# Kernel tuning notes

Measured on AMD Instinct MI355X. Metric: run time of the kernel, lower is better.

The kernel has to match this reference:

```python
import jax, jax.numpy as jnp
import numpy as np

B, N, H, L, V = 512, 20, 450, 56, 780
T = 2 * (N - 1)  # DFS trace length per tree (down+up edge per non-root node)


def _build(rng):
    EpT = 2 * (N - 1)
    n_nodes, n_edges = B * N, B * EpT
    src = np.zeros(n_edges, np.int32); dst = np.zeros(n_edges, np.int32)
    step_eid = np.zeros((T, B), np.int32)
    step_v = np.zeros((T, B), np.int32)
    p_flag = np.zeros((T, B), np.int32)
    for b in range(B):
        par = [0] * N
        ch = [[] for _ in range(N)]
        for i in range(1, N):
            p = int(rng.integers(max(0, i - 3), i))
            par[i] = p; ch[p].append(i)
        eo, no = b * EpT, b * N
        for i in range(1, N):
            d, u = eo + 2 * (i - 1), eo + 2 * (i - 1) + 1
            src[d], dst[d] = no + par[i], no + i
            src[u], dst[u] = no + i, no + par[i]
        trace = []
        stack = [(0, iter(ch[0]))]
        while stack:
            u_, it = stack[-1]
            c = next(it, None)
            if c is None:
                stack.pop()
                if stack:
                    pu = stack[-1][0]
                    trace.append((eo + 2 * (u_ - 1) + 1, no + pu, 0))
            else:
                trace.append((eo + 2 * (c - 1), no + c, 1))
                stack.append((c, iter(ch[c])))
        for t, (e, v, p) in enumerate(trace):
            step_eid[t, b], step_v[t, b], p_flag[t, b] = e, v, p
    return src, dst, step_eid, step_v, p_flag


def setup_inputs() -> dict:
    rng = np.random.default_rng(0)
    src, dst, step_eid, step_v, p_flag = _build(rng)
    n_nodes, n_edges = B * N, B * 2 * (N - 1)
    in_lists = [[] for _ in range(n_nodes)]
    for e in range(n_edges):
        in_lists[dst[e]].append(e)
    Dn = max(len(l) for l in in_lists)
    node_in = np.full((n_nodes, Dn), n_edges, np.int32)  # pad with sentinel n_edges
    for v, l in enumerate(in_lists):
        node_in[v, :len(l)] = l
    # line-graph (non-backtracking) predecessors of edge e=(u,v): edges (w,u), w != v
    preds = [[e2 for e2 in in_lists[src[e]] if src[e2] != dst[e]] for e in range(n_edges)]
    P = max(1, max(len(l) for l in preds))
    edge_pred = np.full((n_edges, P), n_edges, np.int32)
    for e, l in enumerate(preds):
        edge_pred[e, :len(l)] = l
    wid = rng.integers(0, V, n_nodes).astype(np.int32)
    root_ids = (np.arange(B) * N).astype(np.int32)
    # q rows: root block, then per-step rows where node is new (down edges)
    q_rows = list(range(B)); q_tgt = [int(wid[r]) for r in root_ids]
    for t in range(T):
        for b in range(B):
            if p_flag[t, b]:
                q_rows.append((t + 1) * B + b)
                q_tgt.append(int(wid[step_v[t, b]]))
    p_tgt = np.concatenate([p_flag.reshape(-1), np.zeros(B, np.int32)]).astype(np.int32)
    key = jax.random.key(0)
    def W(k, *shape):
        return jax.random.normal(jax.random.fold_in(key, k), shape, jnp.float32) * 0.05
    return dict(
        tree_vec=W(0, B, L), emb=W(1, V, H),
        Wz=W(2, 2 * H, H), bz=jnp.zeros(H, jnp.float32),
        Wh=W(3, 2 * H, H), bh=jnp.zeros(H, jnp.float32),
        Wr=W(4, H, H), Ur=W(5, H, H), br=jnp.zeros(H, jnp.float32),
        Ww=W(6, H + L, H), bw=jnp.zeros(H, jnp.float32),
        Uw=W(7, 2 * H + L, H), bu=jnp.zeros(H, jnp.float32),
        Wo=W(8, H, V), bo=jnp.zeros(V, jnp.float32),
        Us=W(9, H, 1), bs=jnp.zeros(1, jnp.float32),
        wid=jnp.asarray(wid), root_ids=jnp.asarray(root_ids),
        edge_src=jnp.asarray(src), edge_dst=jnp.asarray(dst),
        edge_pred=jnp.asarray(edge_pred), node_in=jnp.asarray(node_in),
        step_eid=jnp.asarray(step_eid), step_v=jnp.asarray(step_v),
        q_rows=jnp.asarray(np.array(q_rows, np.int32)),
        q_tgt=jnp.asarray(np.array(q_tgt, np.int32)),
        p_tgt=jnp.asarray(p_tgt),
    )


def reference(tree_vec, emb, Wz, bz, Wh, bh, Wr, Ur, br, Ww, bw, Uw, bu, Wo, bo, Us, bs,
              wid, root_ids, edge_src, edge_dst, edge_pred, node_in, step_eid, step_v,
              q_rows, q_tgt, p_tgt):
    n_edges = edge_src.shape[0]
    x = emb[wid]                              # [n_nodes, H] node embeddings
    src_x = x[edge_src]; dst_x = x[edge_dst]  # [n_edges, H]
    m0 = jnp.zeros((n_edges + 1, H), x.dtype)  # +1 sentinel zero row for padding

    def step(carry, inp):
        m, rm = carry
        eid, v = inp                          # [B] edge ids / dst node ids this DFS step
        pred = edge_pred[eid]                 # [B, P] non-backtracking predecessor edges
        s = m[pred].sum(1)                    # sum of incoming m
        arm = rm[pred].sum(1)                 # sum of incoming r*m
        sx = src_x[eid]; dx = dst_x[eid]
        z = jax.nn.sigmoid(jnp.concatenate([sx, s], 1) @ Wz + bz)
        m_new = (1 - z) * s + z * jnp.tanh(jnp.concatenate([sx, arm], 1) @ Wh + bh)
        r = jax.nn.sigmoid(dx @ Wr + m_new @ Ur + br)
        m = m.at[eid].set(m_new)
        rm = rm.at[eid].set(r * m_new)
        h = m[node_in[v]].sum(1)              # node pull: h_v = sum of incoming m
        return (m, rm), h

    _, h_steps = jax.lax.scan(step, (m0, m0), (step_eid, step_v))  # [T, B, H]

    x_root = x[root_ids]
    h_root = jnp.zeros_like(x_root)           # roots pulled before any edge update
    x_steps = x[step_v]                        # [T, B, H]
    tv_steps = jnp.broadcast_to(tree_vec[None], (T, B, L))
    p_root = jnp.concatenate([x_root, h_root, tree_vec], 1)[None]
    p_step = jnp.concatenate([x_steps, h_steps, tv_steps], 2)
    p_in = jnp.concatenate([p_root, p_step], 0).reshape((T + 1) * B, 2 * H + L)
    q_root = jnp.concatenate([h_root, tree_vec], 1)[None]
    q_step = jnp.concatenate([h_steps, tv_steps], 2)
    q_in = jnp.concatenate([q_root, q_step], 0).reshape((T + 1) * B, H + L)[q_rows]

    q_logits = jax.nn.relu(q_in @ Ww + bw) @ Wo + bo          # [nq, V]
    p_logit = (jax.nn.relu(p_in @ Uw + bu) @ Us + bs)[:, 0]   # [np]
    tgt = p_tgt.astype(p_logit.dtype)
    p_loss = jnp.sum(jnp.logaddexp(0.0, p_logit) - p_logit * tgt) / B
    lse = jax.nn.logsumexp(q_logits, axis=1)
    q_loss = jnp.sum(lse - jnp.take_along_axis(q_logits, q_tgt[:, None], 1)[:, 0]) / B
    p_acc = jnp.mean(((p_logit > 0).astype(p_tgt.dtype) == p_tgt).astype(jnp.float32))
    q_acc = jnp.mean((jnp.argmax(q_logits, 1).astype(q_tgt.dtype) == q_tgt).astype(jnp.float32))
    return (q_loss, p_loss, q_acc, p_acc)
```

## Files before the change

kernel.cpp:

```cpp
#include <hip/hip_runtime.h>
#include <math.h>

#define B_ 512
#define N_ 20
#define H_ 450
#define L_ 56
#define V_ 780
#define T_ 38
#define NNODES (B_*N_)
#define NEDGES (B_*2*(N_-1))
#define NPROWS ((T_+1)*B_)
#define KS 480
#define NT 4
#define AST 488
#define HSTR 456

typedef __attribute__((ext_vector_type(8))) short bf16x8;
typedef __attribute__((ext_vector_type(4))) float f32x4;

__device__ __forceinline__ float sigmoidf_(float v){ return 1.0f/(1.0f+expf(-v)); }

__device__ __forceinline__ unsigned short f2b(float x){
  unsigned int u = __float_as_uint(x);
  unsigned int r = (u + 0x7fffu + ((u >> 16) & 1u)) >> 16;
  return (unsigned short)r;
}
__device__ __forceinline__ float b2f(unsigned int v){
  return __uint_as_float((v & 0xffffu) << 16);
}
__device__ __forceinline__ unsigned int pack2(float lo, float hi){
  return (unsigned int)f2b(lo) | ((unsigned int)f2b(hi) << 16);
}

__global__ __launch_bounds__(256) void k_gather_xb(const float* __restrict__ emb,
    const int* __restrict__ wid, unsigned short* __restrict__ xb){
  int w = blockIdx.x*4 + (threadIdx.x>>6), lane = threadIdx.x & 63;
  if (w >= NNODES) return;
  const float2* src = (const float2*)(emb + (size_t)wid[w]*H_);
  unsigned int* dst = (unsigned int*)(xb + (size_t)w*KS);
  for (int j2 = lane; j2 < 240; j2 += 64){
    unsigned int v = 0;
    if (j2 < 225){ float2 f = src[j2]; v = pack2(f.x, f.y); }
    dst[j2] = v;
  }
}

__global__ void k_wt(const float* __restrict__ W1, const float* __restrict__ W2,
                     int Ksplit, int Kact, int Nact, unsigned short* __restrict__ dst, int Kpad){
  int c = blockIdx.x;
  unsigned short* drow = dst + (size_t)c*Kpad;
  for (int k = threadIdx.x; k < Kpad; k += blockDim.x){
    float v = 0.f;
    if (c < Nact && k < Kact)
      v = (k < Ksplit) ? W1[(size_t)k*Nact + c] : W2[(size_t)(k-Ksplit)*Nact + c];
    drow[k] = f2b(v);
  }
}

struct ScanP {
  const unsigned short *WzB, *WhB, *UrT;
  const unsigned short *XWz, *XWh, *XWr;
  const int *edge_src, *edge_dst, *step_eid;
  unsigned short *m, *rm;
  unsigned short *hm, *hrm;
  unsigned short *hb;
};

__global__ __launch_bounds__(1024, 4) void k_scan_tree(ScanP p){
  __shared__ unsigned short A1s[16*AST];
  __shared__ unsigned short A2s[16*AST];
  __shared__ unsigned short sZ[NT*HSTR], sH[NT*HSTR], sR[NT*HSTR];
  __shared__ int s_eoff[T_][NT], s_roff[T_][NT], s_srcH[T_][NT], s_dstH[T_][NT];

  const int tid = threadIdx.x;
  const int lane = tid & 63, l15 = lane & 15, kh = lane >> 4, ko = kh*8;
  const int wv = tid >> 6;
  const int r0 = blockIdx.x * NT;
  const int c_0 = wv*32 + l15, c_1 = c_0 + 16;

  const unsigned short* pWz0 = p.WzB + (size_t)c_0*KS;
  const unsigned short* pWz1 = p.WzB + (size_t)c_1*KS;
  const unsigned short* pWh0 = p.WhB + (size_t)c_0*KS;
  const unsigned short* pWh1 = p.WhB + (size_t)c_1*KS;
  const unsigned short* pUr0 = p.UrT + (size_t)c_0*KS;
  const unsigned short* pUr1 = p.UrT + (size_t)c_1*KS;
  const unsigned short* aA1 = A1s + l15*AST;
  const unsigned short* aA2 = A2s + l15*AST;

  for (int idx = tid; idx < 16*AST; idx += 1024){ A1s[idx] = 0; A2s[idx] = 0; }
  for (int idx = tid; idx < T_*NT; idx += 1024){
    int t = idx >> 2, rl = idx & 3;
    int e = p.step_eid[t*B_ + r0 + rl];
    s_eoff[t][rl] = e*KS;
    s_roff[t][rl] = (e ^ 1)*KS;
    s_srcH[t][rl] = p.edge_src[e]*HSTR;
    s_dstH[t][rl] = p.edge_dst[e]*HSTR;
  }
  __syncthreads();

  for (int t = 0; t < T_; ++t){
    bf16x8 bz0[3], bz1[3], bh0[3], bh1[3];
    #pragma unroll
    for (int i = 0; i < 3; ++i){
      bz0[i] = *(const bf16x8*)(pWz0 + i*32 + ko);
      bz1[i] = *(const bf16x8*)(pWz1 + i*32 + ko);
      bh0[i] = *(const bf16x8*)(pWh0 + i*32 + ko);
      bh1[i] = *(const bf16x8*)(pWh1 + i*32 + ko);
    }

    if (tid < 228){
      int rl = tid / 57, g = tid - rl*57;
      int j = g*8;
      uint4 hm4 = *(const uint4*)(p.hm  + s_srcH[t][rl] + j);
      uint4 hr4 = *(const uint4*)(p.hrm + s_srcH[t][rl] + j);
      uint4 mr4 = *(const uint4*)(p.m   + s_roff[t][rl] + j);
      uint4 rr4 = *(const uint4*)(p.rm  + s_roff[t][rl] + j);
      uint4 o1, o2;
      o1.x = pack2(b2f(hm4.x)-b2f(mr4.x), b2f(hm4.x>>16)-b2f(mr4.x>>16));
      o1.y = pack2(b2f(hm4.y)-b2f(mr4.y), b2f(hm4.y>>16)-b2f(mr4.y>>16));
      o1.z = pack2(b2f(hm4.z)-b2f(mr4.z), b2f(hm4.z>>16)-b2f(mr4.z>>16));
      o1.w = pack2(b2f(hm4.w)-b2f(mr4.w), b2f(hm4.w>>16)-b2f(mr4.w>>16));
      o2.x = pack2(b2f(hr4.x)-b2f(rr4.x), b2f(hr4.x>>16)-b2f(rr4.x>>16));
      o2.y = pack2(b2f(hr4.y)-b2f(rr4.y), b2f(hr4.y>>16)-b2f(rr4.y>>16));
      o2.z = pack2(b2f(hr4.z)-b2f(rr4.z), b2f(hr4.z>>16)-b2f(rr4.z>>16));
      o2.w = pack2(b2f(hr4.w)-b2f(rr4.w), b2f(hr4.w>>16)-b2f(rr4.w>>16));
      *(uint4*)(A1s + rl*AST + j) = o1;
      *(uint4*)(A2s + rl*AST + j) = o2;
    } else if (tid < 912){
      int idx2 = tid - 228;
      int mat = idx2 / 228, rem = idx2 - mat*228;
      int rl = rem / 57, g = rem - rl*57;
      int row = (mat == 2) ? s_dstH[t][rl] : s_srcH[t][rl];
      const unsigned short* src = (mat == 0) ? p.XWz : (mat == 1) ? p.XWh : p.XWr;
      unsigned short* d = (mat == 0) ? sZ : (mat == 1) ? sH : sR;
      *(uint4*)(d + rl*HSTR + g*8) = *(const uint4*)(src + row + g*8);
    }
    __syncthreads();

    f32x4 accZ0 = {}, accZ1 = {}, accH0 = {}, accH1 = {};
    #pragma unroll
    for (int it = 0; it < 15; ++it){
      const int sl = it % 3;
      bf16x8 a1 = *(const bf16x8*)(aA1 + it*32 + ko);
      bf16x8 a2 = *(const bf16x8*)(aA2 + it*32 + ko);
      accZ0 = __builtin_amdgcn_mfma_f32_16x16x32_bf16(a1, bz0[sl], accZ0, 0,0,0);
      accZ1 = __builtin_amdgcn_mfma_f32_16x16x32_bf16(a1, bz1[sl], accZ1, 0,0,0);
      accH0 = __builtin_amdgcn_mfma_f32_16x16x32_bf16(a2, bh0[sl], accH0, 0,0,0);
      accH1 = __builtin_amdgcn_mfma_f32_16x16x32_bf16(a2, bh1[sl], accH1, 0,0,0);
      if (it + 3 < 15){
        bz0[sl] = *(const bf16x8*)(pWz0 + (it+3)*32 + ko);
        bz1[sl] = *(const bf16x8*)(pWz1 + (it+3)*32 + ko);
        bh0[sl] = *(const bf16x8*)(pWh0 + (it+3)*32 + ko);
        bh1[sl] = *(const bf16x8*)(pWh1 + (it+3)*32 + ko);
      }
    }
    __syncthreads();

    bf16x8 bu0[3], bu1[3];
    #pragma unroll
    for (int i = 0; i < 3; ++i){
      bu0[i] = *(const bf16x8*)(pUr0 + i*32 + ko);
      bu1[i] = *(const bf16x8*)(pUr1 + i*32 + ko);
    }

    if (kh == 0){
      #pragma unroll
      for (int n = 0; n < 2; ++n){
        int cc = wv*32 + n*16 + l15;
        if (cc < H_){
          f32x4 aZ = n ? accZ1 : accZ0;
          f32x4 aH = n ? accH1 : accH0;
          #pragma unroll
          for (int reg = 0; reg < 4; ++reg){
            int rl = reg;
            float z  = sigmoidf_(aZ[reg] + b2f(sZ[rl*HSTR + cc]));
            float th = tanhf   (aH[reg] + b2f(sH[rl*HSTR + cc]));
            float s_ = b2f(A1s[rl*AST + cc]);
            float mn = (1.f - z)*s_ + z*th;
            unsigned short mb = f2b(mn);
            p.m[s_eoff[t][rl] + cc] = mb;
            A2s[rl*AST + cc] = mb;
            float hv = b2f(p.hm[s_dstH[t][rl] + cc]) + mn;
            p.hm[s_dstH[t][rl] + cc] = f2b(hv);
            p.hb[(size_t)(t*B_ + r0 + rl)*HSTR + cc] = f2b(hv);
          }
        }
      }
    }
    __syncthreads();

    f32x4 accR0 = {}, accR1 = {};
    #pragma unroll
    for (int it = 0; it < 15; ++it){
      const int sl = it % 3;
      bf16x8 a = *(const bf16x8*)(aA2 + it*32 + ko);
      accR0 = __builtin_amdgcn_mfma_f32_16x16x32_bf16(a, bu0[sl], accR0, 0,0,0);
      accR1 = __builtin_amdgcn_mfma_f32_16x16x32_bf16(a, bu1[sl], accR1, 0,0,0);
      if (it + 3 < 15){
        bu0[sl] = *(const bf16x8*)(pUr0 + (it+3)*32 + ko);
        bu1[sl] = *(const bf16x8*)(pUr1 + (it+3)*32 + ko);
      }
    }

    if (kh == 0){
      #pragma unroll
      for (int n = 0; n < 2; ++n){
        int cc = wv*32 + n*16 + l15;
        if (cc < H_){
          f32x4 aR = n ? accR1 : accR0;
          #pragma unroll
          for (int reg = 0; reg < 4; ++reg){
            int rl = reg;
            float r_ = sigmoidf_(aR[reg] + b2f(sR[rl*HSTR + cc]));
            float mn = b2f(A2s[rl*AST + cc]);
            float rv = r_*mn;
            p.rm[s_eoff[t][rl] + cc] = f2b(rv);
            float hv = b2f(p.hrm[s_dstH[t][rl] + cc]) + rv;
            p.hrm[s_dstH[t][rl] + cc] = f2b(hv);
          }
        }
      }
    }
    __syncthreads();
  }
}

__device__ __forceinline__ void mfma_tile_core(
    const unsigned short* __restrict__ A, const unsigned short* __restrict__ BT,
    int K, int gr0, int gc0, int tid,
    unsigned short* __restrict__ As, unsigned short* __restrict__ Bs,
    f32x4 (&acc)[2][2])
{
  const int lane = tid & 63;
  const int w = tid >> 6, wr = w >> 1, wc = w & 1;
  const int l15 = lane & 15, kh = lane >> 4;
  const int sr = tid >> 2, sj = (tid & 3) * 8;
  const size_t arow = (size_t)(gr0 + sr) * K;
  const size_t brow = (size_t)(gc0 + sr) * K;
  for (int kt = 0; kt < K; kt += 32){
    __syncthreads();
    *(float4*)&As[sr*40 + sj] = *(const float4*)&A[arow + kt + sj];
    *(float4*)&Bs[sr*40 + sj] = *(const float4*)&BT[brow + kt + sj];
    __syncthreads();
    bf16x8 a0 = *(const bf16x8*)&As[(wr*32      + l15)*40 + kh*8];
    bf16x8 a1 = *(const bf16x8*)&As[(wr*32 + 16 + l15)*40 + kh*8];
    bf16x8 b0 = *(const bf16x8*)&Bs[(wc*32      + l15)*40 + kh*8];
    bf16x8 b1 = *(const bf16x8*)&Bs[(wc*32 + 16 + l15)*40 + kh*8];
    acc[0][0] = __builtin_amdgcn_mfma_f32_16x16x32_bf16(a0,b0,acc[0][0],0,0,0);
    acc[0][1] = __builtin_amdgcn_mfma_f32_16x16x32_bf16(a0,b1,acc[0][1],0,0,0);
    acc[1][0] = __builtin_amdgcn_mfma_f32_16x16x32_bf16(a1,b0,acc[1][0],0,0,0);
    acc[1][1] = __builtin_amdgcn_mfma_f32_16x16x32_bf16(a1,b1,acc[1][1],0,0,0);
  }
}

__global__ __launch_bounds__(256) void k_head_mfma(
    const unsigned short* __restrict__ A, const unsigned short* __restrict__ BT, int K,
    const float* __restrict__ bias, int Nact, int relu,
    float* __restrict__ outF, int ldF, unsigned short* __restrict__ outB, int ldB)
{
  __shared__ unsigned short As[64*40], Bs[64*40];
  const int tid = threadIdx.x;
  const int gr0 = blockIdx.y*64, gc0 = blockIdx.x*64;
  f32x4 acc[2][2] = {};
  mfma_tile_core(A, BT, K, gr0, gc0, tid, As, Bs, acc);
  const int lane = tid & 63;
  const int w = tid >> 6, wr = w >> 1, wc = w & 1;
  const int l15 = lane & 15, kh = lane >> 4;
  #pragma unroll
  for (int mi = 0; mi < 2; ++mi){
    #pragma unroll
    for (int n = 0; n < 2; ++n){
      int c = gc0 + wc*32 + n*16 + l15;
      float bc = (c < Nact) ? bias[c] : 0.f;
      #pragma unroll
      for (int reg = 0; reg < 4; ++reg){
        int r = gr0 + wr*32 + mi*16 + kh*4 + reg;
        float v = acc[mi][n][reg] + bc;
        if (relu) v = fmaxf(v, 0.f);
        if (outF && c < Nact) outF[(size_t)r*ldF + c] = v;
        if (outB && c < ldB)  outB[(size_t)r*ldB + c] = (c < Nact) ? f2b(v) : (unsigned short)0;
      }
    }
  }
}

__global__ __launch_bounds__(256) void k_head_p(
    const unsigned short* __restrict__ A, const unsigned short* __restrict__ BT,
    const float* __restrict__ bu_, const float* __restrict__ Us, float* __restrict__ plog)
{
  __shared__ unsigned short As[64*40], Bs[64*40];
  const int tid = threadIdx.x;
  const int gr0 = blockIdx.y*64, gc0 = blockIdx.x*64;
  f32x4 acc[2][2] = {};
  mfma_tile_core(A, BT, 960, gr0, gc0, tid, As, Bs, acc);
  const int lane = tid & 63;
  const int w = tid >> 6, wr = w >> 1, wc = w & 1;
  const int l15 = lane & 15, kh = lane >> 4;
  #pragma unroll
  for (int mi = 0; mi < 2; ++mi){
    float rowsum[4] = {0.f,0.f,0.f,0.f};
    #pragma unroll
    for (int n = 0; n < 2; ++n){
      int c = gc0 + wc*32 + n*16 + l15;
      float uc = 0.f, bc = 0.f;
      if (c < H_){ uc = Us[c]; bc = bu_[c]; }
      #pragma unroll
      for (int reg = 0; reg < 4; ++reg){
        float v = fmaxf(acc[mi][n][reg] + bc, 0.f);
        rowsum[reg] += (c < H_) ? v*uc : 0.f;
      }
    }
    #pragma unroll
    for (int reg = 0; reg < 4; ++reg){
      float pv = rowsum[reg];
      pv += __shfl_xor(pv,1); pv += __shfl_xor(pv,2);
      pv += __shfl_xor(pv,4); pv += __shfl_xor(pv,8);
      if (l15 == 0) atomicAdd(plog + gr0 + wr*32 + mi*16 + kh*4 + reg, pv);
    }
  }
}

__global__ __launch_bounds__(256) void k_build_Aq(const unsigned short* __restrict__ hb,
    const float* __restrict__ tv, const int* __restrict__ q_rows,
    unsigned short* __restrict__ Aq, int nq){
  int w = blockIdx.x*4 + (threadIdx.x>>6), lane = threadIdx.x & 63;
  int nw = gridDim.x*4;
  for (int i = w; i < nq; i += nw){
    int row = q_rows[i]; int b = row & (B_-1);
    unsigned short* dst = Aq + (size_t)i*512;
    if (row < B_){
      for (int j2 = lane; j2 < 225; j2 += 64) ((unsigned int*)dst)[j2] = 0u;
    } else {
      const unsigned int* src = (const unsigned int*)(hb + (size_t)(row-B_)*HSTR);
      for (int j2 = lane; j2 < 225; j2 += 64) ((unsigned int*)dst)[j2] = src[j2];
    }
    int k = 450 + lane;
    if (k < 512){
      unsigned short v = 0;
      if (k < 506) v = f2b(tv[b*L_ + (k-450)]);
      dst[k] = v;
    }
  }
}

__global__ __launch_bounds__(256) void k_build_Ap(const unsigned short* __restrict__ hb,
    const unsigned short* __restrict__ xb, const float* __restrict__ tv,
    const int* __restrict__ root_ids, const int* __restrict__ step_v,
    unsigned short* __restrict__ Ap){
  int w = blockIdx.x*4 + (threadIdx.x>>6), lane = threadIdx.x & 63;
  int nw = gridDim.x*4;
  for (int i = w; i < NPROWS; i += nw){
    int b = i & (B_-1);
    unsigned short* dst = Ap + (size_t)i*960;
    int xn = (i < B_) ? root_ids[b] : step_v[i - B_];
    const unsigned int* xr = (const unsigned int*)(xb + (size_t)xn*KS);
    for (int j2 = lane; j2 < 225; j2 += 64) ((unsigned int*)dst)[j2] = xr[j2];
    if (i < B_){
      for (int j2 = lane; j2 < 225; j2 += 64) ((unsigned int*)(dst + 450))[j2] = 0u;
    } else {
      const unsigned int* hr = (const unsigned int*)(hb + (size_t)(i-B_)*HSTR);
      for (int j2 = lane; j2 < 225; j2 += 64) ((unsigned int*)(dst + 450))[j2] = hr[j2];
    }
    int k = 900 + lane;
    if (k < 960){
      unsigned short v = 0;
      if (k < 956) v = f2b(tv[b*L_ + (k-900)]);
      dst[k] = v;
    }
  }
}

__global__ __launch_bounds__(256) void k_qreduce2(const float* __restrict__ logits,
    const int* __restrict__ q_tgt, int nq, float* __restrict__ out){
  int w = blockIdx.x*4 + (threadIdx.x>>6), lane = threadIdx.x & 63;
  int nw = gridDim.x*4;
  float qloss = 0.f, qacc = 0.f;
  for (int i = w; i < nq; i += nw){
    const float4* lr4 = (const float4*)(logits + (size_t)i*V_);
    float4 vals[4]; int cnt = 0;
    float mx = -INFINITY; int mi = 0x7fffffff;
    for (int j4 = lane; j4 < 195; j4 += 64){
      float4 v = lr4[j4]; vals[cnt++] = v;
      #pragma unroll
      for (int u = 0; u < 4; ++u){
        float f = ((float*)&v)[u];
        if (f > mx){ mx = f; mi = j4*4 + u; }
      }
    }
    #pragma unroll
    for (int off = 32; off; off >>= 1){
      float omx = __shfl_xor(mx, off); int omi = __shfl_xor(mi, off);
      if (omx > mx || (omx == mx && omi < mi)){ mx = omx; mi = omi; }
    }
    float ps = 0.f; cnt = 0;
    for (int j4 = lane; j4 < 195; j4 += 64){
      float4 v = vals[cnt++];
      ps += expf(v.x-mx) + expf(v.y-mx) + expf(v.z-mx) + expf(v.w-mx);
    }
    #pragma unroll
    for (int off = 32; off; off >>= 1) ps += __shfl_xor(ps, off);
    if (lane == 0){
      int tg = q_tgt[i];
      float lt = logits[(size_t)i*V_ + tg];
      qloss += mx + logf(ps) - lt;
      qacc  += (mi == tg) ? 1.f : 0.f;
    }
  }
  if (lane == 0){
    atomicAdd(out+0, qloss*(1.0f/B_));
    atomicAdd(out+2, qacc *(1.0f/(float)nq));
  }
}

__global__ __launch_bounds__(256) void k_pfinal(const float* __restrict__ plog,
    const float* __restrict__ bs, const int* __restrict__ p_tgt, float* __restrict__ out){
  int i = blockIdx.x*256 + threadIdx.x;
  float loss = 0.f, acc = 0.f;
  if (i < NPROWS){
    float pl = plog[i] + bs[0];
    float tgt = (float)p_tgt[i];
    loss = fmaxf(pl, 0.f) + log1pf(expf(-fabsf(pl))) - pl*tgt;
    acc = (((pl > 0.f) ? 1 : 0) == p_tgt[i]) ? 1.f : 0.f;
  }
  #pragma unroll
  for (int off = 32; off; off >>= 1){
    loss += __shfl_xor(loss, off); acc += __shfl_xor(acc, off);
  }
  if ((threadIdx.x & 63) == 0){
    atomicAdd(out+1, loss*(1.0f/B_));
    atomicAdd(out+3, acc *(1.0f/(float)NPROWS));
  }
}

extern "C" void kernel_launch(void* const* d_in, const int* in_sizes, int n_in,
                              void* d_out, int out_size, void* d_ws, size_t ws_size,
                              hipStream_t stream){
  const float* tree_vec = (const float*)d_in[0];
  const float* emb  = (const float*)d_in[1];
  const float* Wz   = (const float*)d_in[2];
  const float* bz   = (const float*)d_in[3];
  const float* Wh   = (const float*)d_in[4];
  const float* bh   = (const float*)d_in[5];
  const float* Wr   = (const float*)d_in[6];
  const float* Ur   = (const float*)d_in[7];
  const float* br   = (const float*)d_in[8];
  const float* Ww   = (const float*)d_in[9];
  const float* bw   = (const float*)d_in[10];
  const float* Uw   = (const float*)d_in[11];
  const float* bu   = (const float*)d_in[12];
  const float* Wo   = (const float*)d_in[13];
  const float* bo   = (const float*)d_in[14];
  const float* Us   = (const float*)d_in[15];
  const float* bs   = (const float*)d_in[16];
  const int* wid      = (const int*)d_in[17];
  const int* root_ids = (const int*)d_in[18];
  const int* edge_src = (const int*)d_in[19];
  const int* edge_dst = (const int*)d_in[20];
  const int* step_eid = (const int*)d_in[23];
  const int* step_v   = (const int*)d_in[24];
  const int* q_rows   = (const int*)d_in[25];
  const int* q_tgt    = (const int*)d_in[26];
  const int* p_tgt    = (const int*)d_in[27];
  int nq = in_sizes[25];

  char* ws = (char*)d_ws;
  const size_t XB_OFF    = 0;
  const size_t HB_OFF    = 9830400;
  const size_t M_OFF     = 27574272;
  const size_t RM_OFF    = M_OFF + 18678784;
  const size_t HM_OFF    = RM_OFF + 18678784;
  const size_t HRM_OFF   = HM_OFF + 9338880;
  const size_t WZB_OFF   = HRM_OFF + 9338880;
  const size_t WHB_OFF   = WZB_OFF + 491520;
  const size_t URT_OFF   = WHB_OFF + 491520;
  const size_t WZTOP_OFF = URT_OFF + 491520;
  const size_t WHTOP_OFF = WZTOP_OFF + 491520;
  const size_t WRT_OFF   = WHTOP_OFF + 491520;
  const size_t WWT_OFF   = WRT_OFF + 491520;
  const size_t UWT_OFF   = WWT_OFF + 524288;
  const size_t WOT_OFF   = UWT_OFF + 983040;
  const size_t XWZ_OFF   = WOT_OFF + 851968;
  const size_t XWH_OFF   = XWZ_OFF + 9338880;
  const size_t XWR_OFF   = XWH_OFF + 9338880;
  const size_t LQ_OFF  = M_OFF;
  const size_t AQ_OFF  = XWZ_OFF;
  const size_t HQB_OFF = AQ_OFF + 10485760;
  const size_t PL_OFF  = HQB_OFF + 10485760;
  const size_t AP_OFF  = M_OFF;

  unsigned short* xb = (unsigned short*)(ws + XB_OFF);
  unsigned short* hb = (unsigned short*)(ws + HB_OFF);
  unsigned short* m_ = (unsigned short*)(ws + M_OFF);
  unsigned short* rm = (unsigned short*)(ws + RM_OFF);
  unsigned short* hm = (unsigned short*)(ws + HM_OFF);
  unsigned short* hrm = (unsigned short*)(ws + HRM_OFF);
  unsigned short* WzB = (unsigned short*)(ws + WZB_OFF);
  unsigned short* WhB = (unsigned short*)(ws + WHB_OFF);
  unsigned short* UrT = (unsigned short*)(ws + URT_OFF);
  unsigned short* WzTop = (unsigned short*)(ws + WZTOP_OFF);
  unsigned short* WhTop = (unsigned short*)(ws + WHTOP_OFF);
  unsigned short* WrT = (unsigned short*)(ws + WRT_OFF);
  unsigned short* WwT = (unsigned short*)(ws + WWT_OFF);
  unsigned short* UwT = (unsigned short*)(ws + UWT_OFF);
  unsigned short* WoT = (unsigned short*)(ws + WOT_OFF);
  unsigned short* XWz = (unsigned short*)(ws + XWZ_OFF);
  unsigned short* XWh = (unsigned short*)(ws + XWH_OFF);
  unsigned short* XWr = (unsigned short*)(ws + XWR_OFF);

  hipMemsetAsync(ws + M_OFF, 0, 2*18678784ull + 2*9338880ull, stream);
  hipMemsetAsync(d_out, 0, (size_t)out_size*sizeof(float), stream);

  k_gather_xb<<<2560, 256, 0, stream>>>(emb, wid, xb);

  k_wt<<<512, 256, 0, stream>>>(Wz + 450*450, Wz, 450, 450, 450, WzB, KS);
  k_wt<<<512, 256, 0, stream>>>(Wh + 450*450, Wh, 450, 450, 450, WhB, KS);
  k_wt<<<512, 256, 0, stream>>>(Ur, Ur, 450, 450, 450, UrT, KS);
  k_wt<<<512, 256, 0, stream>>>(Wz, Wz, 450, 450, 450, WzTop, KS);
  k_wt<<<512, 256, 0, stream>>>(Wh, Wh, 450, 450, 450, WhTop, KS);
  k_wt<<<512, 256, 0, stream>>>(Wr, Wr, 450, 450, 450, WrT, KS);
  k_wt<<<512, 256, 0, stream>>>(Ww, Ww, 506, 506, 450, WwT, 512);
  k_wt<<<512, 256, 0, stream>>>(Uw, Uw, 956, 956, 450, UwT, 960);
  k_wt<<<832, 256, 0, stream>>>(Wo, Wo, 450, 450, 780, WoT, 512);

  k_head_mfma<<<dim3(8,160), 256, 0, stream>>>(xb, WzTop, KS, bz, H_, 0, nullptr, 0, XWz, HSTR);
  k_head_mfma<<<dim3(8,160), 256, 0, stream>>>(xb, WhTop, KS, bh, H_, 0, nullptr, 0, XWh, HSTR);
  k_head_mfma<<<dim3(8,160), 256, 0, stream>>>(xb, WrT,   KS, br, H_, 0, nullptr, 0, XWr, HSTR);

  ScanP sp;
  sp.WzB = WzB; sp.WhB = WhB; sp.UrT = UrT;
  sp.XWz = XWz; sp.XWh = XWh; sp.XWr = XWr;
  sp.edge_src = edge_src; sp.edge_dst = edge_dst; sp.step_eid = step_eid;
  sp.m = m_; sp.rm = rm; sp.hm = hm; sp.hrm = hrm; sp.hb = hb;
  k_scan_tree<<<B_/NT, 1024, 0, stream>>>(sp);

  unsigned short* Aq  = (unsigned short*)(ws + AQ_OFF);
  float* logitsq      = (float*)(ws + LQ_OFF);
  unsigned short* hqb = (unsigned short*)(ws + HQB_OFF);
  float* plog         = (float*)(ws + PL_OFF);
  hipMemsetAsync(plog, 0, (size_t)NPROWS*4, stream);

  k_build_Aq<<<640, 256, 0, stream>>>(hb, tree_vec, q_rows, Aq, nq);
  k_head_mfma<<<dim3(8, nq/64), 256, 0, stream>>>(Aq, WwT, 512, bw, H_, 1,
      nullptr, 0, hqb, 512);
  k_head_mfma<<<dim3(13, nq/64), 256, 0, stream>>>(hqb, WoT, 512, bo, V_, 0,
      logitsq, V_, nullptr, 0);
  k_qreduce2<<<320, 256, 0, stream>>>(logitsq, q_tgt, nq, (float*)d_out);

  unsigned short* Ap = (unsigned short*)(ws + AP_OFF);
  k_build_Ap<<<1248, 256, 0, stream>>>(hb, xb, tree_vec, root_ids, step_v, Ap);
  k_head_p<<<dim3(8, NPROWS/64), 256, 0, stream>>>(Ap, UwT, bu, Us, plog);
  k_pfinal<<<78, 256, 0, stream>>>(plog, bs, p_tgt, (float*)d_out);
}
```

Before: 1.352 ms.

## Fuse weight transposes, xW GEMMs, and A-matrix gathers; bf16 logits; triple-buffer scan

```diff
diff --git a/kernel.cpp b/kernel.cpp
--- a/kernel.cpp
+++ b/kernel.cpp
@@ -14,6 +14,9 @@
 #define NT 4
 #define AST 488
 #define HSTR 456
+#define KQ 512
+#define KPP 992
+#define LDL 784
 
 typedef __attribute__((ext_vector_type(8))) short bf16x8;
 typedef __attribute__((ext_vector_type(4))) float f32x4;
@@ -45,15 +48,69 @@
   }
 }
 
-__global__ void k_wt(const float* __restrict__ W1, const float* __restrict__ W2,
-                     int Ksplit, int Kact, int Nact, unsigned short* __restrict__ dst, int Kpad){
-  int c = blockIdx.x;
-  unsigned short* drow = dst + (size_t)c*Kpad;
-  for (int k = threadIdx.x; k < Kpad; k += blockDim.x){
-    float v = 0.f;
-    if (c < Nact && k < Kact)
-      v = (k < Ksplit) ? W1[(size_t)k*Nact + c] : W2[(size_t)(k-Ksplit)*Nact + c];
-    drow[k] = f2b(v);
+__global__ void k_wtall(const float* __restrict__ Wz, const float* __restrict__ Wh,
+    const float* __restrict__ Ur, const float* __restrict__ Wr,
+    const float* __restrict__ Ww, const float* __restrict__ Uw,
+    const float* __restrict__ Wo, const float* __restrict__ tv,
+    unsigned short* __restrict__ WzB, unsigned short* __restrict__ WhB,
+    unsigned short* __restrict__ UrT, unsigned short* __restrict__ WzTop,
+    unsigned short* __restrict__ WhTop, unsigned short* __restrict__ WrT,
+    unsigned short* __restrict__ WwT, unsigned short* __restrict__ UwT,
+    unsigned short* __restrict__ WoT, unsigned short* __restrict__ tvb){
+  int bid = blockIdx.x;
+  if (bid < 512*6){
+    int seg = bid >> 9, c = bid & 511;
+    const float* src; unsigned short* dst; int rowbase;
+    switch(seg){
+      case 0: src = Wz; dst = WzB; rowbase = 450; break;
+      case 1: src = Wh; dst = WhB; rowbase = 450; break;
+      case 2: src = Ur; dst = UrT; rowbase = 0; break;
+      case 3: src = Wz; dst = WzTop; rowbase = 0; break;
+      case 4: src = Wh; dst = WhTop; rowbase = 0; break;
+      default: src = Wr; dst = WrT; rowbase = 0; break;
+    }
+    unsigned short* drow = dst + (size_t)c*KS;
+    for (int k = threadIdx.x; k < KS; k += blockDim.x){
+      float v = 0.f;
+      if (c < 450 && k < 450) v = src[(size_t)(rowbase + k)*450 + c];
+      drow[k] = f2b(v);
+    }
+  } else if (bid < 512*7){
+    int c = bid - 512*6;
+    unsigned short* drow = WwT + (size_t)c*KQ;
+    for (int k = threadIdx.x; k < KQ; k += blockDim.x){
+      float v = 0.f;
+      if (c < 450){
+        if (k < 450) v = Ww[(size_t)k*450 + c];
+        else if (k >= 456) v = Ww[(size_t)(450 + k - 456)*450 + c];
+      }
+      drow[k] = f2b(v);
+    }
+  } else if (bid < 512*8){
+    int c = bid - 512*7;
+    unsigned short* drow = UwT + (size_t)c*KPP;
+    for (int k = threadIdx.x; k < KPP; k += blockDim.x){
+      float v = 0.f;
+      if (c < 450){
+        if (k < 450) v = Uw[(size_t)k*450 + c];
+        else if (k >= 480 && k < 930) v = Uw[(size_t)(450 + k - 480)*450 + c];
+        else if (k >= 936) v = Uw[(size_t)(900 + k - 936)*450 + c];
+      }
+      drow[k] = f2b(v);
+    }
+  } else if (bid < 512*8 + 832){
+    int c = bid - 512*8;
+    unsigned short* drow = WoT + (size_t)c*512;
+    for (int k = threadIdx.x; k < 512; k += blockDim.x){
+      float v = 0.f;
+      if (c < V_ && k < 450) v = Wo[(size_t)k*V_ + c];
+      drow[k] = f2b(v);
+    }
+  } else {
+    int b = bid - (512*8 + 832);
+    unsigned short* drow = tvb + (size_t)b*64;
+    for (int k = threadIdx.x; k < 64; k += blockDim.x)
+      drow[k] = f2b((k < L_) ? tv[b*L_ + k] : 0.f);
   }
 }
 
@@ -69,6 +126,7 @@
 __global__ __launch_bounds__(1024, 4) void k_scan_tree(ScanP p){
   __shared__ unsigned short A1s[16*AST];
   __shared__ unsigned short A2s[16*AST];
+  __shared__ unsigned short A3s[16*AST];
   __shared__ unsigned short sZ[NT*HSTR], sH[NT*HSTR], sR[NT*HSTR];
   __shared__ int s_eoff[T_][NT], s_roff[T_][NT], s_srcH[T_][NT], s_dstH[T_][NT];
 
@@ -86,8 +144,9 @@
   const unsigned short* pUr1 = p.UrT + (size_t)c_1*KS;
   const unsigned short* aA1 = A1s + l15*AST;
   const unsigned short* aA2 = A2s + l15*AST;
-
-  for (int idx = tid; idx < 16*AST; idx += 1024){ A1s[idx] = 0; A2s[idx] = 0; }
+  const unsigned short* aA3 = A3s + l15*AST;
+
+  for (int idx = tid; idx < 16*AST; idx += 1024){ A1s[idx] = 0; A2s[idx] = 0; A3s[idx] = 0; }
   for (int idx = tid; idx < T_*NT; idx += 1024){
     int t = idx >> 2, rl = idx & 3;
     int e = p.step_eid[t*B_ + r0 + rl];
@@ -154,7 +213,6 @@
         bh1[sl] = *(const bf16x8*)(pWh1 + (it+3)*32 + ko);
       }
     }
-    __syncthreads();
 
     bf16x8 bu0[3], bu1[3];
     #pragma unroll
@@ -179,7 +237,7 @@
             float mn = (1.f - z)*s_ + z*th;
             unsigned short mb = f2b(mn);
             p.m[s_eoff[t][rl] + cc] = mb;
-            A2s[rl*AST + cc] = mb;
+            A3s[rl*AST + cc] = mb;
             float hv = b2f(p.hm[s_dstH[t][rl] + cc]) + mn;
             p.hm[s_dstH[t][rl] + cc] = f2b(hv);
             p.hb[(size_t)(t*B_ + r0 + rl)*HSTR + cc] = f2b(hv);
@@ -193,7 +251,7 @@
     #pragma unroll
     for (int it = 0; it < 15; ++it){
       const int sl = it % 3;
-      bf16x8 a = *(const bf16x8*)(aA2 + it*32 + ko);
+      bf16x8 a = *(const bf16x8*)(aA3 + it*32 + ko);
       accR0 = __builtin_amdgcn_mfma_f32_16x16x32_bf16(a, bu0[sl], accR0, 0,0,0);
       accR1 = __builtin_amdgcn_mfma_f32_16x16x32_bf16(a, bu1[sl], accR1, 0,0,0);
       if (it + 3 < 15){
@@ -212,7 +270,7 @@
           for (int reg = 0; reg < 4; ++reg){
             int rl = reg;
             float r_ = sigmoidf_(aR[reg] + b2f(sR[rl*HSTR + cc]));
-            float mn = b2f(A2s[rl*AST + cc]);
+            float mn = b2f(A3s[rl*AST + cc]);
             float rv = r_*mn;
             p.rm[s_eoff[t][rl] + cc] = f2b(rv);
             float hv = b2f(p.hrm[s_dstH[t][rl] + cc]) + rv;
@@ -225,22 +283,23 @@
   }
 }
 
-__device__ __forceinline__ void mfma_tile_core(
-    const unsigned short* __restrict__ A, const unsigned short* __restrict__ BT,
-    int K, int gr0, int gc0, int tid,
-    unsigned short* __restrict__ As, unsigned short* __restrict__ Bs,
-    f32x4 (&acc)[2][2])
+__global__ __launch_bounds__(256) void k_head_mfma(
+    const unsigned short* __restrict__ A, const unsigned short* __restrict__ BT, int K,
+    const float* __restrict__ bias, int Nact, int relu,
+    float* __restrict__ outF, int ldF, unsigned short* __restrict__ outB, int ldB)
 {
+  __shared__ unsigned short As[64*40], Bs[64*40];
+  const int tid = threadIdx.x;
+  const int gr0 = blockIdx.y*64, gc0 = blockIdx.x*64;
   const int lane = tid & 63;
   const int w = tid >> 6, wr = w >> 1, wc = w & 1;
   const int l15 = lane & 15, kh = lane >> 4;
   const int sr = tid >> 2, sj = (tid & 3) * 8;
-  const size_t arow = (size_t)(gr0 + sr) * K;
-  const size_t brow = (size_t)(gc0 + sr) * K;
+  f32x4 acc[2][2] = {};
   for (int kt = 0; kt < K; kt += 32){
     __syncthreads();
-    *(float4*)&As[sr*40 + sj] = *(const float4*)&A[arow + kt + sj];
-    *(float4*)&Bs[sr*40 + sj] = *(const float4*)&BT[brow + kt + sj];
+    *(float4*)&As[sr*40 + sj] = *(const float4*)&A[(size_t)(gr0+sr)*K + kt + sj];
+    *(float4*)&Bs[sr*40 + sj] = *(const float4*)&BT[(size_t)(gc0+sr)*K + kt + sj];
     __syncthreads();
     bf16x8 a0 = *(const bf16x8*)&As[(wr*32      + l15)*40 + kh*8];
     bf16x8 a1 = *(const bf16x8*)&As[(wr*32 + 16 + l15)*40 + kh*8];
@@ -251,21 +310,6 @@
     acc[1][0] = __builtin_amdgcn_mfma_f32_16x16x32_bf16(a1,b0,acc[1][0],0,0,0);
     acc[1][1] = __builtin_amdgcn_mfma_f32_16x16x32_bf16(a1,b1,acc[1][1],0,0,0);
   }
-}
-
-__global__ __launch_bounds__(256) void k_head_mfma(
-    const unsigned short* __restrict__ A, const unsigned short* __restrict__ BT, int K,
-    const float* __restrict__ bias, int Nact, int relu,
-    float* __restrict__ outF, int ldF, unsigned short* __restrict__ outB, int ldB)
-{
-  __shared__ unsigned short As[64*40], Bs[64*40];
-  const int tid = threadIdx.x;
-  const int gr0 = blockIdx.y*64, gc0 = blockIdx.x*64;
-  f32x4 acc[2][2] = {};
-  mfma_tile_core(A, BT, K, gr0, gc0, tid, As, Bs, acc);
-  const int lane = tid & 63;
-  const int w = tid >> 6, wr = w >> 1, wc = w & 1;
-  const int l15 = lane & 15, kh = lane >> 4;
   #pragma unroll
   for (int mi = 0; mi < 2; ++mi){
     #pragma unroll
@@ -284,18 +328,160 @@
   }
 }
 
-__global__ __launch_bounds__(256) void k_head_p(
-    const unsigned short* __restrict__ A, const unsigned short* __restrict__ BT,
-    const float* __restrict__ bu_, const float* __restrict__ Us, float* __restrict__ plog)
+__global__ __launch_bounds__(256) void k_xw(const unsigned short* __restrict__ xb,
+    const unsigned short* __restrict__ WzTop, const unsigned short* __restrict__ WhTop,
+    const unsigned short* __restrict__ WrT,
+    const float* __restrict__ bz, const float* __restrict__ bh, const float* __restrict__ br,
+    unsigned short* __restrict__ XWz, unsigned short* __restrict__ XWh,
+    unsigned short* __restrict__ XWr)
 {
   __shared__ unsigned short As[64*40], Bs[64*40];
+  const unsigned short* BT = (blockIdx.z == 0) ? WzTop : (blockIdx.z == 1) ? WhTop : WrT;
+  const float* bias        = (blockIdx.z == 0) ? bz    : (blockIdx.z == 1) ? bh    : br;
+  unsigned short* outB     = (blockIdx.z == 0) ? XWz   : (blockIdx.z == 1) ? XWh   : XWr;
   const int tid = threadIdx.x;
   const int gr0 = blockIdx.y*64, gc0 = blockIdx.x*64;
-  f32x4 acc[2][2] = {};
-  mfma_tile_core(A, BT, 960, gr0, gc0, tid, As, Bs, acc);
   const int lane = tid & 63;
   const int w = tid >> 6, wr = w >> 1, wc = w & 1;
   const int l15 = lane & 15, kh = lane >> 4;
+  const int sr = tid >> 2, sj = (tid & 3) * 8;
+  f32x4 acc[2][2] = {};
+  for (int kt = 0; kt < KS; kt += 32){
+    __syncthreads();
+    *(float4*)&As[sr*40 + sj] = *(const float4*)&xb[(size_t)(gr0+sr)*KS + kt + sj];
+    *(float4*)&Bs[sr*40 + sj] = *(const float4*)&BT[(size_t)(gc0+sr)*KS + kt + sj];
+    __syncthreads();
+    bf16x8 a0 = *(const bf16x8*)&As[(wr*32      + l15)*40 + kh*8];
+    bf16x8 a1 = *(const bf16x8*)&As[(wr*32 + 16 + l15)*40 + kh*8];
+    bf16x8 b0 = *(const bf16x8*)&Bs[(wc*32      + l15)*40 + kh*8];
+    bf16x8 b1 = *(const bf16x8*)&Bs[(wc*32 + 16 + l15)*40 + kh*8];
+    acc[0][0] = __builtin_amdgcn_mfma_f32_16x16x32_bf16(a0,b0,acc[0][0],0,0,0);
+    acc[0][1] = __builtin_amdgcn_mfma_f32_16x16x32_bf16(a0,b1,acc[0][1],0,0,0);
+    acc[1][0] = __builtin_amdgcn_mfma_f32_16x16x32_bf16(a1,b0,acc[1][0],0,0,0);
+    acc[1][1] = __builtin_amdgcn_mfma_f32_16x16x32_bf16(a1,b1,acc[1][1],0,0,0);
+  }
+  #pragma unroll
+  for (int mi = 0; mi < 2; ++mi){
+    #pragma unroll
+    for (int n = 0; n < 2; ++n){
+      int c = gc0 + wc*32 + n*16 + l15;
+      if (c >= HSTR) continue;
+      float bc = (c < H_) ? bias[c] : 0.f;
+      #pragma unroll
+      for (int reg = 0; reg < 4; ++reg){
+        int r = gr0 + wr*32 + mi*16 + kh*4 + reg;
+        outB[(size_t)r*HSTR + c] = (c < H_) ? f2b(acc[mi][n][reg] + bc) : (unsigned short)0;
+      }
+    }
+  }
+}
+
+__global__ __launch_bounds__(256) void k_head_q(const unsigned short* __restrict__ hb,
+    const unsigned short* __restrict__ tvb, const int* __restrict__ q_rows,
+    const unsigned short* __restrict__ BT, const float* __restrict__ bw,
+    unsigned short* __restrict__ hqb, int nq)
+{
+  __shared__ unsigned short As[64*40], Bs[64*40];
+  __shared__ int s_hrow[64], s_b[64];
+  const int tid = threadIdx.x;
+  const int gr0 = blockIdx.y*64, gc0 = blockIdx.x*64;
+  if (tid < 64){
+    int gi = gr0 + tid;
+    int row = (gi < nq) ? q_rows[gi] : 0;
+    s_hrow[tid] = (row < B_) ? -1 : row - B_;
+    s_b[tid] = row & (B_-1);
+  }
+  const int lane = tid & 63;
+  const int w = tid >> 6, wr = w >> 1, wc = w & 1;
+  const int l15 = lane & 15, kh = lane >> 4;
+  const int sr = tid >> 2, sj = (tid & 3) * 8;
+  f32x4 acc[2][2] = {};
+  for (int kt = 0; kt < KQ; kt += 32){
+    __syncthreads();
+    int gk = kt + sj;
+    uint4 av;
+    if (gk < 456){
+      int hr = s_hrow[sr];
+      if (hr < 0){ av.x = av.y = av.z = av.w = 0u; }
+      else av = *(const uint4*)(hb + (size_t)hr*HSTR + gk);
+    } else {
+      av = *(const uint4*)(tvb + (size_t)s_b[sr]*64 + (gk - 456));
+    }
+    *(uint4*)&As[sr*40 + sj] = av;
+    *(float4*)&Bs[sr*40 + sj] = *(const float4*)&BT[(size_t)(gc0+sr)*KQ + gk];
+    __syncthreads();
+    bf16x8 a0 = *(const bf16x8*)&As[(wr*32      + l15)*40 + kh*8];
+    bf16x8 a1 = *(const bf16x8*)&As[(wr*32 + 16 + l15)*40 + kh*8];
+    bf16x8 b0 = *(const bf16x8*)&Bs[(wc*32      + l15)*40 + kh*8];
+    bf16x8 b1 = *(const bf16x8*)&Bs[(wc*32 + 16 + l15)*40 + kh*8];
+    acc[0][0] = __builtin_amdgcn_mfma_f32_16x16x32_bf16(a0,b0,acc[0][0],0,0,0);
+    acc[0][1] = __builtin_amdgcn_mfma_f32_16x16x32_bf16(a0,b1,acc[0][1],0,0,0);
+    acc[1][0] = __builtin_amdgcn_mfma_f32_16x16x32_bf16(a1,b0,acc[1][0],0,0,0);
+    acc[1][1] = __builtin_amdgcn_mfma_f32_16x16x32_bf16(a1,b1,acc[1][1],0,0,0);
+  }
+  #pragma unroll
+  for (int mi = 0; mi < 2; ++mi){
+    #pragma unroll
+    for (int n = 0; n < 2; ++n){
+      int c = gc0 + wc*32 + n*16 + l15;
+      float bc = (c < H_) ? bw[c] : 0.f;
+      #pragma unroll
+      for (int reg = 0; reg < 4; ++reg){
+        int r = gr0 + wr*32 + mi*16 + kh*4 + reg;
+        float v = fmaxf(acc[mi][n][reg] + bc, 0.f);
+        hqb[(size_t)r*KQ + c] = (c < H_) ? f2b(v) : (unsigned short)0;
+      }
+    }
+  }
+}
+
+__global__ __launch_bounds__(256) void k_head_p2(const unsigned short* __restrict__ xb,
+    const unsigned short* __restrict__ hb, const unsigned short* __restrict__ tvb,
+    const int* __restrict__ root_ids, const int* __restrict__ step_v,
+    const unsigned short* __restrict__ BT, const float* __restrict__ bu_,
+    const float* __restrict__ Us, float* __restrict__ plog)
+{
+  __shared__ unsigned short As[64*40], Bs[64*40];
+  __shared__ int s_xrow[64], s_hrow[64], s_b[64];
+  const int tid = threadIdx.x;
+  const int gr0 = blockIdx.y*64, gc0 = blockIdx.x*64;
+  if (tid < 64){
+    int i = gr0 + tid;
+    int b = i & (B_-1);
+    s_b[tid] = b;
+    s_xrow[tid] = (i < B_) ? root_ids[b] : step_v[i - B_];
+    s_hrow[tid] = (i < B_) ? -1 : i - B_;
+  }
+  const int lane = tid & 63;
+  const int w = tid >> 6, wr = w >> 1, wc = w & 1;
+  const int l15 = lane & 15, kh = lane >> 4;
+  const int sr = tid >> 2, sj = (tid & 3) * 8;
+  f32x4 acc[2][2] = {};
+  for (int kt = 0; kt < KPP; kt += 32){
+    __syncthreads();
+    int gk = kt + sj;
+    uint4 av;
+    if (gk < 480){
+      av = *(const uint4*)(xb + (size_t)s_xrow[sr]*KS + gk);
+    } else if (gk < 936){
+      int hr = s_hrow[sr];
+      if (hr < 0){ av.x = av.y = av.z = av.w = 0u; }
+      else av = *(const uint4*)(hb + (size_t)hr*HSTR + (gk - 480));
+    } else {
+      av = *(const uint4*)(tvb + (size_t)s_b[sr]*64 + (gk - 936));
+    }
+    *(uint4*)&As[sr*40 + sj] = av;
+    *(float4*)&Bs[sr*40 + sj] = *(const float4*)&BT[(size_t)(gc0+sr)*KPP + gk];
+    __syncthreads();
+    bf16x8 a0 = *(const bf16x8*)&As[(wr*32      + l15)*40 + kh*8];
+    bf16x8 a1 = *(const bf16x8*)&As[(wr*32 + 16 + l15)*40 + kh*8];
+    bf16x8 b0 = *(const bf16x8*)&Bs[(wc*32      + l15)*40 + kh*8];
+    bf16x8 b1 = *(const bf16x8*)&Bs[(wc*32 + 16 + l15)*40 + kh*8];
+    acc[0][0] = __builtin_amdgcn_mfma_f32_16x16x32_bf16(a0,b0,acc[0][0],0,0,0);
+    acc[0][1] = __builtin_amdgcn_mfma_f32_16x16x32_bf16(a0,b1,acc[0][1],0,0,0);
+    acc[1][0] = __builtin_amdgcn_mfma_f32_16x16x32_bf16(a1,b0,acc[1][0],0,0,0);
+    acc[1][1] = __builtin_amdgcn_mfma_f32_16x16x32_bf16(a1,b1,acc[1][1],0,0,0);
+  }
   #pragma unroll
   for (int mi = 0; mi < 2; ++mi){
     float rowsum[4] = {0.f,0.f,0.f,0.f};
@@ -320,72 +506,22 @@
   }
 }
 
-__global__ __launch_bounds__(256) void k_build_Aq(const unsigned short* __restrict__ hb,
-    const float* __restrict__ tv, const int* __restrict__ q_rows,
-    unsigned short* __restrict__ Aq, int nq){
-  int w = blockIdx.x*4 + (threadIdx.x>>6), lane = threadIdx.x & 63;
-  int nw = gridDim.x*4;
-  for (int i = w; i < nq; i += nw){
-    int row = q_rows[i]; int b = row & (B_-1);
-    unsigned short* dst = Aq + (size_t)i*512;
-    if (row < B_){
-      for (int j2 = lane; j2 < 225; j2 += 64) ((unsigned int*)dst)[j2] = 0u;
-    } else {
-      const unsigned int* src = (const unsigned int*)(hb + (size_t)(row-B_)*HSTR);
-      for (int j2 = lane; j2 < 225; j2 += 64) ((unsigned int*)dst)[j2] = src[j2];
-    }
-    int k = 450 + lane;
-    if (k < 512){
-      unsigned short v = 0;
-      if (k < 506) v = f2b(tv[b*L_ + (k-450)]);
-      dst[k] = v;
-    }
-  }
-}
-
-__global__ __launch_bounds__(256) void k_build_Ap(const unsigned short* __restrict__ hb,
-    const unsigned short* __restrict__ xb, const float* __restrict__ tv,
-    const int* __restrict__ root_ids, const int* __restrict__ step_v,
-    unsigned short* __restrict__ Ap){
-  int w = blockIdx.x*4 + (threadIdx.x>>6), lane = threadIdx.x & 63;
-  int nw = gridDim.x*4;
-  for (int i = w; i < NPROWS; i += nw){
-    int b = i & (B_-1);
-    unsigned short* dst = Ap + (size_t)i*960;
-    int xn = (i < B_) ? root_ids[b] : step_v[i - B_];
-    const unsigned int* xr = (const unsigned int*)(xb + (size_t)xn*KS);
-    for (int j2 = lane; j2 < 225; j2 += 64) ((unsigned int*)dst)[j2] = xr[j2];
-    if (i < B_){
-      for (int j2 = lane; j2 < 225; j2 += 64) ((unsigned int*)(dst + 450))[j2] = 0u;
-    } else {
-      const unsigned int* hr = (const unsigned int*)(hb + (size_t)(i-B_)*HSTR);
-      for (int j2 = lane; j2 < 225; j2 += 64) ((unsigned int*)(dst + 450))[j2] = hr[j2];
-    }
-    int k = 900 + lane;
-    if (k < 960){
-      unsigned short v = 0;
-      if (k < 956) v = f2b(tv[b*L_ + (k-900)]);
-      dst[k] = v;
-    }
-  }
-}
-
-__global__ __launch_bounds__(256) void k_qreduce2(const float* __restrict__ logits,
+__global__ __launch_bounds__(256) void k_qreduce3(const unsigned short* __restrict__ logits,
     const int* __restrict__ q_tgt, int nq, float* __restrict__ out){
   int w = blockIdx.x*4 + (threadIdx.x>>6), lane = threadIdx.x & 63;
   int nw = gridDim.x*4;
   float qloss = 0.f, qacc = 0.f;
   for (int i = w; i < nq; i += nw){
-    const float4* lr4 = (const float4*)(logits + (size_t)i*V_);
-    float4 vals[4]; int cnt = 0;
+    const uint2* lr2 = (const uint2*)(logits + (size_t)i*LDL);
+    uint2 vals[4]; int cnt = 0;
     float mx = -INFINITY; int mi = 0x7fffffff;
     for (int j4 = lane; j4 < 195; j4 += 64){
-      float4 v = lr4[j4]; vals[cnt++] = v;
-      #pragma unroll
-      for (int u = 0; u < 4; ++u){
-        float f = ((float*)&v)[u];
-        if (f > mx){ mx = f; mi = j4*4 + u; }
-      }
+      uint2 v = lr2[j4]; vals[cnt++] = v;
+      float e0 = b2f(v.x), e1 = b2f(v.x>>16), e2 = b2f(v.y), e3 = b2f(v.y>>16);
+      if (e0 > mx){ mx = e0; mi = j4*4; }
+      if (e1 > mx){ mx = e1; mi = j4*4+1; }
+      if (e2 > mx){ mx = e2; mi = j4*4+2; }
+      if (e3 > mx){ mx = e3; mi = j4*4+3; }
     }
     #pragma unroll
     for (int off = 32; off; off >>= 1){
@@ -394,14 +530,15 @@
     }
     float ps = 0.f; cnt = 0;
     for (int j4 = lane; j4 < 195; j4 += 64){
-      float4 v = vals[cnt++];
-      ps += expf(v.x-mx) + expf(v.y-mx) + expf(v.z-mx) + expf(v.w-mx);
+      uint2 v = vals[cnt++];
+      ps += expf(b2f(v.x)-mx) + expf(b2f(v.x>>16)-mx)
+          + expf(b2f(v.y)-mx) + expf(b2f(v.y>>16)-mx);
     }
     #pragma unroll
     for (int off = 32; off; off >>= 1) ps += __shfl_xor(ps, off);
     if (lane == 0){
       int tg = q_tgt[i];
-      float lt = logits[(size_t)i*V_ + tg];
+      float lt = b2f((unsigned int)logits[(size_t)i*LDL + tg]);
       qloss += mx + logf(ps) - lt;
       qacc  += (mi == tg) ? 1.f : 0.f;
     }
@@ -478,15 +615,14 @@
   const size_t WRT_OFF   = WHTOP_OFF + 491520;
   const size_t WWT_OFF   = WRT_OFF + 491520;
   const size_t UWT_OFF   = WWT_OFF + 524288;
-  const size_t WOT_OFF   = UWT_OFF + 983040;
-  const size_t XWZ_OFF   = WOT_OFF + 851968;
+  const size_t WOT_OFF   = UWT_OFF + 1015808;
+  const size_t TVB_OFF   = WOT_OFF + 851968;
+  const size_t XWZ_OFF   = TVB_OFF + 65536;
   const size_t XWH_OFF   = XWZ_OFF + 9338880;
   const size_t XWR_OFF   = XWH_OFF + 9338880;
   const size_t LQ_OFF  = M_OFF;
-  const size_t AQ_OFF  = XWZ_OFF;
-  const size_t HQB_OFF = AQ_OFF + 10485760;
-  const size_t PL_OFF  = HQB_OFF + 10485760;
-  const size_t AP_OFF  = M_OFF;
+  const size_t HQB_OFF = XWZ_OFF;
+  const size_t PL_OFF  = XWH_OFF;
 
   unsigned short* xb = (unsigned short*)(ws + XB_OFF);
   unsigned short* hb = (unsigned short*)(ws + HB_OFF);
@@ -503,28 +639,18 @@
   unsigned short* WwT = (unsigned short*)(ws + WWT_OFF);
   unsigned short* UwT = (unsigned short*)(ws + UWT_OFF);
   unsigned short* WoT = (unsigned short*)(ws + WOT_OFF);
+  unsigned short* tvb = (unsigned short*)(ws + TVB_OFF);
   unsigned short* XWz = (unsigned short*)(ws + XWZ_OFF);
   unsigned short* XWh = (unsigned short*)(ws + XWH_OFF);
   unsigned short* XWr = (unsigned short*)(ws + XWR_OFF);
 
-  hipMemsetAsync(ws + M_OFF, 0, 2*18678784ull + 2*9338880ull, stream);
+  hipMemsetAsync(ws + HB_OFF, 0, WZB_OFF - HB_OFF, stream);
   hipMemsetAsync(d_out, 0, (size_t)out_size*sizeof(float), stream);
 
   k_gather_xb<<<2560, 256, 0, stream>>>(emb, wid, xb);
-
-  k_wt<<<512, 256, 0, stream>>>(Wz + 450*450, Wz, 450, 450, 450, WzB, KS);
-  k_wt<<<512, 256, 0, stream>>>(Wh + 450*450, Wh, 450, 450, 450, WhB, KS);
-  k_wt<<<512, 256, 0, stream>>>(Ur, Ur, 450, 450, 450, UrT, KS);
-  k_wt<<<512, 256, 0, stream>>>(Wz, Wz, 450, 450, 450, WzTop, KS);
-  k_wt<<<512, 256, 0, stream>>>(Wh, Wh, 450, 450, 450, WhTop, KS);
-  k_wt<<<512, 256, 0, stream>>>(Wr, Wr, 450, 450, 450, WrT, KS);
-  k_wt<<<512, 256, 0, stream>>>(Ww, Ww, 506, 506, 450, WwT, 512);
-  k_wt<<<512, 256, 0, stream>>>(Uw, Uw, 956, 956, 450, UwT, 960);
-  k_wt<<<832, 256, 0, stream>>>(Wo, Wo, 450, 450, 780, WoT, 512);
-
-  k_head_mfma<<<dim3(8,160), 256, 0, stream>>>(xb, WzTop, KS, bz, H_, 0, nullptr, 0, XWz, HSTR);
-  k_head_mfma<<<dim3(8,160), 256, 0, stream>>>(xb, WhTop, KS, bh, H_, 0, nullptr, 0, XWh, HSTR);
-  k_head_mfma<<<dim3(8,160), 256, 0, stream>>>(xb, WrT,   KS, br, H_, 0, nullptr, 0, XWr, HSTR);
+  k_wtall<<<512*8 + 832 + 512, 256, 0, stream>>>(Wz, Wh, Ur, Wr, Ww, Uw, Wo, tree_vec,
+      WzB, WhB, UrT, WzTop, WhTop, WrT, WwT, UwT, WoT, tvb);
+  k_xw<<<dim3(8,160,3), 256, 0, stream>>>(xb, WzTop, WhTop, WrT, bz, bh, br, XWz, XWh, XWr);
 
   ScanP sp;
   sp.WzB = WzB; sp.WhB = WhB; sp.UrT = UrT;
@@ -533,21 +659,17 @@
   sp.m = m_; sp.rm = rm; sp.hm = hm; sp.hrm = hrm; sp.hb = hb;
   k_scan_tree<<<B_/NT, 1024, 0, stream>>>(sp);
 
-  unsigned short* Aq  = (unsigned short*)(ws + AQ_OFF);
-  float* logitsq      = (float*)(ws + LQ_OFF);
-  unsigned short* hqb = (unsigned short*)(ws + HQB_OFF);
-  float* plog         = (float*)(ws + PL_OFF);
+  unsigned short* logitsq = (unsigned short*)(ws + LQ_OFF);
+  unsigned short* hqb     = (unsigned short*)(ws + HQB_OFF);
+  float* plog             = (float*)(ws + PL_OFF);
   hipMemsetAsync(plog, 0, (size_t)NPROWS*4, stream);
 
-  k_build_Aq<<<640, 256, 0, stream>>>(hb, tree_vec, q_rows, Aq, nq);
-  k_head_mfma<<<dim3(8, nq/64), 256, 0, stream>>>(Aq, WwT, 512, bw, H_, 1,
-      nullptr, 0, hqb, 512);
+  k_head_q<<<dim3(8, nq/64), 256, 0, stream>>>(hb, tvb, q_rows, WwT, bw, hqb, nq);
   k_head_mfma<<<dim3(13, nq/64), 256, 0, stream>>>(hqb, WoT, 512, bo, V_, 0,
-      logitsq, V_, nullptr, 0);
-  k_qreduce2<<<320, 256, 0, stream>>>(logitsq, q_tgt, nq, (float*)d_out);
-
-  unsigned short* Ap = (unsigned short*)(ws + AP_OFF);
-  k_build_Ap<<<1248, 256, 0, stream>>>(hb, xb, tree_vec, root_ids, step_v, Ap);
-  k_head_p<<<dim3(8, NPROWS/64), 256, 0, stream>>>(Ap, UwT, bu, Us, plog);
+      nullptr, 0, logitsq, LDL);
+  k_qreduce3<<<320, 256, 0, stream>>>(logitsq, q_tgt, nq, (float*)d_out);
+
+  k_head_p2<<<dim3(8, NPROWS/64), 256, 0, stream>>>(xb, hb, tvb, root_ids, step_v,
+      UwT, bu, Us, plog);
   k_pfinal<<<78, 256, 0, stream>>>(plog, bs, p_tgt, (float*)d_out);
 }
```

New measurement: 1.322 ms. 1.02x faster.
